# Kernel tuning notes

Measured on AMD Instinct MI355X. Metric: run time of the kernel, lower is better.

## Reference

```python
import jax, jax.numpy as jnp
import numpy as np

B, F, H, C, K, NHID = 4096, 512, 1024, 100, 32, 3  # NHID = num_layers - 1 hidden->hidden layers


def setup_inputs() -> dict:
    key = jax.random.key(0)
    ks = jax.random.split(key, 5)
    s_in = 1.0 / np.sqrt(F)
    s_h = 1.0 / np.sqrt(H)
    return {
        "x": jax.random.normal(ks[0], (B, F), dtype=jnp.float32),
        "W_in": jax.random.normal(ks[1], (K, F, H), dtype=jnp.float32) * s_in,
        "b_in": jnp.zeros((K, H), dtype=jnp.float32),
        "W_hid": jax.random.normal(ks[2], (NHID, K, H, H), dtype=jnp.float32) * s_h,
        "b_hid": jnp.zeros((NHID, K, H), dtype=jnp.float32),
        "W_out": jax.random.normal(ks[3], (K, H, C), dtype=jnp.float32) * s_h,
        "b_out": jnp.zeros((K, C), dtype=jnp.float32),
    }


def reference(x, W_in, b_in, W_hid, b_hid, W_out, b_out):
    # Batched ensemble: all k MLPs as stacked GEMMs. Dropout off (inference).
    h = jax.nn.relu(jnp.einsum("bf,kfh->kbh", x, W_in) + b_in[:, None, :])  # [K,B,H]
    for i in range(W_hid.shape[0]):  # small fixed layer loop
        h = jax.nn.relu(jnp.einsum("kbh,khj->kbj", h, W_hid[i]) + b_hid[i][:, None, :])
    logits = jnp.einsum("kbh,khc->kbc", h, W_out) + b_out[:, None, :]  # [K,B,C]
    return jnp.mean(logits, axis=0)  # [B,C]
```

## Files before the change

### kernel.cpp

```cpp
#include <hip/hip_runtime.h>
#include <stdint.h>

#define BB   4096
#define FF   512
#define HH   1024
#define CC   100
#define KE   32
#define NHIDL 3
#define CPAD 128

typedef __attribute__((ext_vector_type(8))) short short8;
typedef __attribute__((ext_vector_type(4))) float float4_t;

__device__ __forceinline__ unsigned short f2h(float f) {
  _Float16 h = (_Float16)f;
  union { _Float16 h; unsigned short u; } cv;
  cv.h = h;
  return cv.u;
}

__device__ __forceinline__ void gll16(const void* g, void* l) {
  __builtin_amdgcn_global_load_lds((const __attribute__((address_space(1))) void*)g,
                                   (__attribute__((address_space(3))) void*)l,
                                   16, 0, 0);
}

__global__ void cvt_f16(const float* __restrict__ in, unsigned short* __restrict__ out, int n4) {
  int i = blockIdx.x * 256 + threadIdx.x;
  if (i < n4) {
    float4 v = ((const float4*)in)[i];
    ushort4 o;
    o.x = f2h(v.x); o.y = f2h(v.y); o.z = f2h(v.z); o.w = f2h(v.w);
    ((ushort4*)out)[i] = o;
  }
}

__global__ void transpose_cvt(const float* __restrict__ in, unsigned short* __restrict__ out,
                              int R, int C, int Cpad) {
  __shared__ float tile[32][33];
  int b = blockIdx.z;
  const float* ib = in + (size_t)b * R * C;
  unsigned short* ob = out + (size_t)b * Cpad * R;
  int c0 = blockIdx.x * 32, r0 = blockIdx.y * 32;
  int tx = threadIdx.x & 31, ty = threadIdx.x >> 5;
#pragma unroll
  for (int j = 0; j < 4; ++j) {
    int r = r0 + ty + j * 8, c = c0 + tx;
    tile[ty + j * 8][tx] = (c < C) ? ib[(size_t)r * C + c] : 0.0f;
  }
  __syncthreads();
#pragma unroll
  for (int j = 0; j < 4; ++j) {
    int orow = c0 + ty + j * 8, ocol = r0 + tx;
    if (orow < Cpad) ob[(size_t)orow * R + ocol] = f2h(tile[tx][ty + j * 8]);
  }
}

__global__ void reduce_mean(const float* __restrict__ L, float* __restrict__ out,
                            int n, long long sk) {
  int i = blockIdx.x * 256 + threadIdx.x;
  if (i < n) {
    float s = 0.f;
#pragma unroll
    for (int k = 0; k < KE; ++k) s += L[(long long)k * sk + i];
    out[i] = s * (1.0f / (float)KE);
  }
}

template <int RELU, int FINAL, int KD>
__global__ __launch_bounds__(256, 4) void gemm_f16(
    const unsigned short* __restrict__ A, long long sAk,
    const unsigned short* __restrict__ Bt, long long sBk,
    const float* __restrict__ bias, int sBiasK,
    unsigned short* __restrict__ Out, long long sOutK,
    float* __restrict__ OutF, long long sFk) {
  const int t = threadIdx.x;
  const int lane = t & 63;
  const int wave = t >> 6;
  const int wm = wave & 1;
  const int wn = wave >> 1;
  const int kz = blockIdx.z;
  const int m0 = blockIdx.y * 128;
  const int n0 = blockIdx.x * 128;

  const unsigned short* Ab = A + (long long)kz * sAk + (long long)m0 * KD;
  const unsigned short* Bb = Bt + (long long)kz * sBk + (long long)n0 * KD;

  __shared__ __align__(16) unsigned short smA[128 * 64];
  __shared__ __align__(16) unsigned short smB[128 * 64];

  float4_t acc[4][4];
#pragma unroll
  for (int i = 0; i < 4; ++i)
#pragma unroll
    for (int j = 0; j < 4; ++j) acc[i][j] = (float4_t){0.f, 0.f, 0.f, 0.f};

  int goff[4];
  unsigned short* la[4];
  unsigned short* lb[4];
#pragma unroll
  for (int j = 0; j < 4; ++j) {
    int s = j * 256 + t;
    int row = s >> 3;
    int g = (s & 7) ^ (row & 7);
    goff[j] = row * KD + g * 8;
    la[j] = smA + (size_t)((j * 256 + (t & 0xC0)) * 8);
    lb[j] = smB + (size_t)((j * 256 + (t & 0xC0)) * 8);
  }

  const int r16 = lane & 15;
  const int q = lane >> 4;
  int offA[4][2], offB[4][2];
#pragma unroll
  for (int i = 0; i < 4; ++i) {
#pragma unroll
    for (int kh = 0; kh < 2; ++kh) {
      int ra = wm * 64 + i * 16 + r16;
      offA[i][kh] = ra * 64 + ((((kh * 4 + q)) ^ (ra & 7)) << 3);
      int rb = wn * 64 + i * 16 + r16;
      offB[i][kh] = rb * 64 + ((((kh * 4 + q)) ^ (rb & 7)) << 3);
    }
  }

#pragma unroll
  for (int kt = 0; kt < KD; kt += 64) {
#pragma unroll
    for (int j = 0; j < 4; ++j) gll16(Ab + goff[j] + kt, la[j]);
#pragma unroll
    for (int j = 0; j < 4; ++j) gll16(Bb + goff[j] + kt, lb[j]);
    __syncthreads();

#pragma unroll
    for (int kh = 0; kh < 2; ++kh) {
      short8 af[4], bf[4];
#pragma unroll
      for (int i = 0; i < 4; ++i) af[i] = *(const short8*)(smA + offA[i][kh]);
#pragma unroll
      for (int i = 0; i < 4; ++i) bf[i] = *(const short8*)(smB + offB[i][kh]);
#pragma unroll
      for (int mi = 0; mi < 4; ++mi)
#pragma unroll
        for (int ni = 0; ni < 4; ++ni)
          acc[mi][ni] = __builtin_amdgcn_mfma_f32_16x16x32_f16(af[mi], bf[ni], acc[mi][ni], 0, 0, 0);
    }
    __syncthreads();
  }

  const int rbase = q * 4;
  if (FINAL) {
#pragma unroll
    for (int ni = 0; ni < 4; ++ni) {
      int n = wn * 64 + ni * 16 + r16;
      if (n < CC) {
        float bv = bias[kz * sBiasK + n];
#pragma unroll
        for (int mi = 0; mi < 4; ++mi) {
#pragma unroll
          for (int r = 0; r < 4; ++r) {
            int m = m0 + wm * 64 + mi * 16 + rbase + r;
            OutF[(long long)kz * sFk + (long long)m * CC + n] = acc[mi][ni][r] + bv;
          }
        }
      }
    }
  } else {
#pragma unroll
    for (int ni = 0; ni < 4; ++ni) {
      int n = n0 + wn * 64 + ni * 16 + r16;
      float bv = bias[kz * sBiasK + n];
#pragma unroll
      for (int mi = 0; mi < 4; ++mi) {
        int m = m0 + wm * 64 + mi * 16 + rbase;
        unsigned short* op = Out + (long long)kz * sOutK + (long long)m * HH + n;
#pragma unroll
        for (int r = 0; r < 4; ++r) {
          float v = acc[mi][ni][r] + bv;
          if (RELU) v = fmaxf(v, 0.f);
          op[(long long)r * HH] = f2h(v);
        }
      }
    }
  }
}

extern "C" void kernel_launch(void* const* d_in, const int* in_sizes, int n_in,
                              void* d_out, int out_size, void* d_ws, size_t ws_size,
                              hipStream_t stream) {
  (void)in_sizes; (void)n_in; (void)out_size;
  const float* x     = (const float*)d_in[0];
  const float* W_in  = (const float*)d_in[1];
  const float* b_in  = (const float*)d_in[2];
  const float* W_hid = (const float*)d_in[3];
  const float* b_hid = (const float*)d_in[4];
  const float* W_out = (const float*)d_in[5];
  const float* b_out = (const float*)d_in[6];
  float* out = (float*)d_out;

  char* ws = (char*)d_ws;
  size_t off = 0;
  auto alloc = [&](size_t bytes) -> void* {
    void* p = ws + off;
    off += (bytes + 255) & ~(size_t)255;
    return p;
  };
  unsigned short* xb    = (unsigned short*)alloc((size_t)BB * FF * 2);
  unsigned short* WinT  = (unsigned short*)alloc((size_t)KE * HH * FF * 2);
  unsigned short* WhidT = (unsigned short*)alloc((size_t)NHIDL * KE * HH * HH * 2);
  unsigned short* WoutT = (unsigned short*)alloc((size_t)KE * CPAD * HH * 2);
  size_t fixed = off;

  int Bc = BB;
  while (Bc > 128 && fixed + 2 * (size_t)KE * Bc * HH * 2 > ws_size) Bc >>= 1;
  unsigned short* h0 = (unsigned short*)alloc((size_t)KE * Bc * HH * 2);
  unsigned short* h1 = (unsigned short*)alloc((size_t)KE * Bc * HH * 2);

  cvt_f16<<<(BB * FF / 4 + 255) / 256, 256, 0, stream>>>(x, xb, BB * FF / 4);
  transpose_cvt<<<dim3(HH / 32, FF / 32, KE), 256, 0, stream>>>(W_in, WinT, FF, HH, HH);
  transpose_cvt<<<dim3(HH / 32, HH / 32, NHIDL * KE), 256, 0, stream>>>(W_hid, WhidT, HH, HH, HH);
  transpose_cvt<<<dim3(CPAD / 32, HH / 32, KE), 256, 0, stream>>>(W_out, WoutT, HH, CC, CPAD);

  for (int c0 = 0; c0 < BB; c0 += Bc) {
    gemm_f16<1, 0, FF><<<dim3(HH / 128, Bc / 128, KE), 256, 0, stream>>>(
        xb + (size_t)c0 * FF, 0LL, WinT, (long long)HH * FF, b_in, HH,
        h0, (long long)Bc * HH, nullptr, 0LL);
    unsigned short* hin = h0;
    unsigned short* hout = h1;
    for (int l = 0; l < NHIDL; ++l) {
      gemm_f16<1, 0, HH><<<dim3(HH / 128, Bc / 128, KE), 256, 0, stream>>>(
          hin, (long long)Bc * HH, WhidT + (size_t)l * KE * HH * HH, (long long)HH * HH,
          b_hid + (size_t)l * KE * HH, HH, hout, (long long)Bc * HH, nullptr, 0LL);
      unsigned short* tmp = hin; hin = hout; hout = tmp;
    }
    float* Lbuf = (float*)hout;
    gemm_f16<0, 1, HH><<<dim3(1, Bc / 128, KE), 256, 0, stream>>>(
        hin, (long long)Bc * HH, WoutT, (long long)CPAD * HH, b_out, CC,
        nullptr, 0LL, Lbuf, (long long)Bc * CC);
    reduce_mean<<<(Bc * CC + 255) / 256, 256, 0, stream>>>(
        Lbuf, out + (size_t)c0 * CC, Bc * CC, (long long)Bc * CC);
  }
}
```

Baseline: 1.957 ms.

## Add 256x256-tile double-buffered pipelined GEMM for input and hidden layers

Adds a new 512-thread GEMM kernel with 256x256 output tiles, two LDS buffers staged via global_load_lds, and a hand-scheduled interleave of LDS reads, async loads and MFMA quarters. It uses explicit waitcnt/barriers, setprio around MFMA blocks, and an XCD-aware block remap. It targets the old kernel's lack of load/compute overlap and its low arithmetic intensity per tile. In exchange it uses 128KB of LDS and a large accumulator array, which limits occupancy, and the hand-written sync schedule is fragile. It is used for the input and hidden layers when the batch chunk is a multiple of 256.

```diff
diff --git a/kernel.cpp b/kernel.cpp
--- a/kernel.cpp
+++ b/kernel.cpp
@@ -183,6 +183,146 @@
   }
 }
 
+template <int RELU, int KD>
+__global__ __launch_bounds__(512, 2) void gemm256(
+    const unsigned short* __restrict__ A, long long sAk,
+    const unsigned short* __restrict__ Bt, long long sBk,
+    const float* __restrict__ bias, int sBiasK,
+    unsigned short* __restrict__ Out, long long sOutK) {
+  static_assert(KD % 128 == 0, "need even K-tile count");
+  const int t = threadIdx.x;
+  const int lane = t & 63;
+  const int wave = t >> 6;
+  const int wm = wave >> 2;
+  const int wn = wave & 3;
+  const int r16 = lane & 15;
+  const int q = lane >> 4;
+
+  const int gx = gridDim.x, gy = gridDim.y;
+  const int gxy = gx * gy;
+  const int nwg = gxy * gridDim.z;
+  int flat = blockIdx.x + gx * (blockIdx.y + gy * blockIdx.z);
+  int id2 = (flat & 7) * (nwg >> 3) + (flat >> 3);
+  const int kz = id2 / gxy;
+  int rem = id2 - kz * gxy;
+  const int ty = rem / gx;
+  const int tx = rem - ty * gx;
+  const int m0 = ty * 256;
+  const int n0 = tx * 256;
+
+  const unsigned short* Ab = A + (long long)kz * sAk + (long long)m0 * KD;
+  const unsigned short* Bb = Bt + (long long)kz * sBk + (long long)n0 * KD;
+
+  __shared__ __align__(16) unsigned short sm[2 * 32768];
+
+  const int gq = (t >> 3) * KD + ((((t & 7) ^ ((t >> 3) & 7))) << 3);
+  const int wbase = wave * 512;
+
+  const int x7 = r16 & 7;
+  const int xk0 = (q ^ x7) << 3;
+  const int xk1 = ((4 + q) ^ x7) << 3;
+  const int baseA = (wm * 128 + r16) * 64;
+  const int baseB = (wn * 64 + r16) * 64;
+
+  float4_t acc[8][4];
+#pragma unroll
+  for (int i = 0; i < 8; ++i)
+#pragma unroll
+    for (int j = 0; j < 4; ++j) acc[i][j] = (float4_t){0.f, 0.f, 0.f, 0.f};
+
+  short8 af[4][2];
+  short8 bf[4][2];
+
+#define STGA(BUF, QI, TT) gll16(Ab + (QI) * 64 * KD + (TT) * 64 + gq, \
+                                sm + (BUF) * 32768 + (QI) * 4096 + wbase)
+#define STGB(BUF, QI, TT) gll16(Bb + (QI) * 64 * KD + (TT) * 64 + gq, \
+                                sm + (BUF) * 32768 + 16384 + (QI) * 4096 + wbase)
+#define DSA(BUF, MH) do { \
+    const unsigned short* pA_ = sm + (BUF) * 32768 + baseA + (MH) * 4096; \
+    _Pragma("unroll") for (int i_ = 0; i_ < 4; ++i_) { \
+      af[i_][0] = *(const short8*)(pA_ + i_ * 1024 + xk0); \
+      af[i_][1] = *(const short8*)(pA_ + i_ * 1024 + xk1); \
+    } } while (0)
+#define DSB(BUF, NH) do { \
+    const unsigned short* pB_ = sm + (BUF) * 32768 + 16384 + baseB + (NH) * 2048; \
+    _Pragma("unroll") for (int i_ = 0; i_ < 2; ++i_) { \
+      bf[(NH) * 2 + i_][0] = *(const short8*)(pB_ + i_ * 1024 + xk0); \
+      bf[(NH) * 2 + i_][1] = *(const short8*)(pB_ + i_ * 1024 + xk1); \
+    } } while (0)
+#define MM(MH, NH) do { \
+    __builtin_amdgcn_s_setprio(1); \
+    _Pragma("unroll") for (int mi_ = 0; mi_ < 4; ++mi_) { \
+      _Pragma("unroll") for (int ni_ = 0; ni_ < 2; ++ni_) { \
+        acc[(MH) * 4 + mi_][(NH) * 2 + ni_] = __builtin_amdgcn_mfma_f32_16x16x32_f16( \
+            af[mi_][0], bf[(NH) * 2 + ni_][0], acc[(MH) * 4 + mi_][(NH) * 2 + ni_], 0, 0, 0); \
+        acc[(MH) * 4 + mi_][(NH) * 2 + ni_] = __builtin_amdgcn_mfma_f32_16x16x32_f16( \
+            af[mi_][1], bf[(NH) * 2 + ni_][1], acc[(MH) * 4 + mi_][(NH) * 2 + ni_], 0, 0, 0); \
+      } } \
+    __builtin_amdgcn_s_setprio(0); } while (0)
+#define BAR() __builtin_amdgcn_s_barrier()
+#define VMCNT(n) asm volatile("s_waitcnt vmcnt(" #n ")" ::: "memory")
+#define LGKM0() do { asm volatile("s_waitcnt lgkmcnt(0)" ::: "memory"); \
+                     __builtin_amdgcn_sched_barrier(0); } while (0)
+
+  STGA(0, 0, 0); STGA(0, 1, 0); STGA(0, 2, 0); STGA(0, 3, 0);
+  STGB(0, 0, 0); STGB(0, 1, 0); STGB(0, 2, 0); STGB(0, 3, 0);
+  STGA(1, 0, 1); STGA(1, 2, 1);
+  STGB(1, 0, 1); STGB(1, 1, 1); STGB(1, 2, 1); STGB(1, 3, 1);
+  VMCNT(6);
+  BAR();
+
+  const int nT = KD / 64;
+  const int nI = nT / 2;
+#pragma unroll 1
+  for (int j = 0; j < nI - 1; ++j) {
+    const int O1 = 2 * j + 1, E2 = 2 * j + 2, O2 = 2 * j + 3;
+    DSA(0, 0); DSB(0, 0); STGA(1, 1, O1); STGA(1, 3, O1); BAR(); LGKM0(); MM(0, 0); BAR();
+    DSB(0, 1);            STGA(0, 0, E2); STGA(0, 2, E2); BAR(); LGKM0(); MM(0, 1); BAR();
+    DSA(0, 1);            STGB(0, 0, E2); STGB(0, 1, E2); BAR(); LGKM0(); MM(1, 1); BAR();
+                          STGB(0, 2, E2); STGB(0, 3, E2); VMCNT(6); BAR(); MM(1, 0); BAR();
+    DSA(1, 0); DSB(1, 0); STGA(0, 1, E2); STGA(0, 3, E2); BAR(); LGKM0(); MM(0, 0); BAR();
+    DSB(1, 1);            STGA(1, 0, O2); STGA(1, 2, O2); BAR(); LGKM0(); MM(0, 1); BAR();
+    DSA(1, 1);            STGB(1, 0, O2); STGB(1, 1, O2); BAR(); LGKM0(); MM(1, 1); BAR();
+                          STGB(1, 2, O2); STGB(1, 3, O2); VMCNT(6); BAR(); MM(1, 0); BAR();
+  }
+  {
+    const int O1 = nT - 1;
+    DSA(0, 0); DSB(0, 0); STGA(1, 1, O1); STGA(1, 3, O1); BAR(); LGKM0(); MM(0, 0); BAR();
+    DSB(0, 1); BAR(); LGKM0(); MM(0, 1); BAR();
+    DSA(0, 1); BAR(); LGKM0(); MM(1, 1); BAR();
+    VMCNT(0); BAR(); MM(1, 0); BAR();
+    DSA(1, 0); DSB(1, 0); BAR(); LGKM0(); MM(0, 0); BAR();
+    DSB(1, 1); BAR(); LGKM0(); MM(0, 1); BAR();
+    DSA(1, 1); LGKM0(); MM(1, 1); MM(1, 0);
+  }
+
+  const int rbase = q * 4;
+#pragma unroll
+  for (int ni = 0; ni < 4; ++ni) {
+    const int n = n0 + wn * 64 + ni * 16 + r16;
+    const float bv = bias[kz * sBiasK + n];
+#pragma unroll
+    for (int mi = 0; mi < 8; ++mi) {
+      const int m = m0 + wm * 128 + mi * 16 + rbase;
+      unsigned short* op = Out + (long long)kz * sOutK + (long long)m * HH + n;
+#pragma unroll
+      for (int rr = 0; rr < 4; ++rr) {
+        float v = acc[mi][ni][rr] + bv;
+        if (RELU) v = fmaxf(v, 0.f);
+        op[(long long)rr * HH] = f2h(v);
+      }
+    }
+  }
+#undef STGA
+#undef STGB
+#undef DSA
+#undef DSB
+#undef MM
+#undef BAR
+#undef VMCNT
+#undef LGKM0
+}
+
 extern "C" void kernel_launch(void* const* d_in, const int* in_sizes, int n_in,
                               void* d_out, int out_size, void* d_ws, size_t ws_size,
                               hipStream_t stream) {
@@ -219,16 +359,30 @@
   transpose_cvt<<<dim3(HH / 32, HH / 32, NHIDL * KE), 256, 0, stream>>>(W_hid, WhidT, HH, HH, HH);
   transpose_cvt<<<dim3(CPAD / 32, HH / 32, KE), 256, 0, stream>>>(W_out, WoutT, HH, CC, CPAD);
 
+  const bool big = (Bc % 256) == 0;
+
   for (int c0 = 0; c0 < BB; c0 += Bc) {
-    gemm_f16<1, 0, FF><<<dim3(HH / 128, Bc / 128, KE), 256, 0, stream>>>(
-        xb + (size_t)c0 * FF, 0LL, WinT, (long long)HH * FF, b_in, HH,
-        h0, (long long)Bc * HH, nullptr, 0LL);
+    if (big) {
+      gemm256<1, FF><<<dim3(HH / 256, Bc / 256, KE), 512, 0, stream>>>(
+          xb + (size_t)c0 * FF, 0LL, WinT, (long long)HH * FF, b_in, HH,
+          h0, (long long)Bc * HH);
+    } else {
+      gemm_f16<1, 0, FF><<<dim3(HH / 128, Bc / 128, KE), 256, 0, stream>>>(
+          xb + (size_t)c0 * FF, 0LL, WinT, (long long)HH * FF, b_in, HH,
+          h0, (long long)Bc * HH, nullptr, 0LL);
+    }
     unsigned short* hin = h0;
     unsigned short* hout = h1;
     for (int l = 0; l < NHIDL; ++l) {
-      gemm_f16<1, 0, HH><<<dim3(HH / 128, Bc / 128, KE), 256, 0, stream>>>(
-          hin, (long long)Bc * HH, WhidT + (size_t)l * KE * HH * HH, (long long)HH * HH,
-          b_hid + (size_t)l * KE * HH, HH, hout, (long long)Bc * HH, nullptr, 0LL);
+      if (big) {
+        gemm256<1, HH><<<dim3(HH / 256, Bc / 256, KE), 512, 0, stream>>>(
+            hin, (long long)Bc * HH, WhidT + (size_t)l * KE * HH * HH, (long long)HH * HH,
+            b_hid + (size_t)l * KE * HH, HH, hout, (long long)Bc * HH);
+      } else {
+        gemm_f16<1, 0, HH><<<dim3(HH / 128, Bc / 128, KE), 256, 0, stream>>>(
+            hin, (long long)Bc * HH, WhidT + (size_t)l * KE * HH * HH, (long long)HH * HH,
+            b_hid + (size_t)l * KE * HH, HH, hout, (long long)Bc * HH, nullptr, 0LL);
+      }
       unsigned short* tmp = hin; hin = hout; hout = tmp;
     }
     float* Lbuf = (float*)hout;
```

After: 1.687 ms. 1.16x faster.
